# Optimization experiments

Measured on AMD Instinct MI355X. Metric: run time of the kernel, lower is better.

The kernel has to match this reference:

```python
import jax, jax.numpy as jnp
import numpy as np
import math

D_MODEL = 1024
N_HEADS = 16
HEAD_DIM = D_MODEL // N_HEADS
MLP_DIM = 4 * D_MODEL
B, L, M = 2, 2048, 2048


def layer_norm(x, g, b, eps=1e-5):
    mu = jnp.mean(x, axis=-1, keepdims=True)
    var = jnp.var(x, axis=-1, keepdims=True)
    return (x - mu) * jax.lax.rsqrt(var + eps) * g + b


def mha(q_in, k_in, qW, wW, oW, mask=None):
    # Faithful to source: k and v share w_proj, and the value einsum uses k.
    b, l, _ = q_in.shape
    m = k_in.shape[1]
    q = (q_in @ qW).reshape(b, l, HEAD_DIM, N_HEADS)
    k = (k_in @ wW).reshape(b, m, HEAD_DIM, N_HEADS)
    s = jnp.einsum('bldn,bmdn->blmn', q, k)
    if mask is not None:
        s = jnp.where(mask, -1e9, s)  # mask applied BEFORE scaling, as in source
    s = s / math.sqrt(HEAD_DIM)
    w = jax.nn.softmax(s, axis=2)
    x = jnp.einsum('blmn,bmdn->bldn', w, k)  # source bug: uses k, not v
    x = x.reshape(b, l, HEAD_DIM * N_HEADS)
    return x @ oW


def setup_inputs() -> dict:
    key = jax.random.key(0)
    ks = jax.random.split(key, 16)
    sc = 1.0 / math.sqrt(D_MODEL)
    inp = {
        'x': jax.random.normal(ks[0], (B, L, D_MODEL), jnp.float32),
        'enc_output': jax.random.normal(ks[1], (B, M, D_MODEL), jnp.float32),
        'mask': jax.random.randint(ks[2], (B, 1, M, 1), 0, 2).astype(bool),
        'q1W': jax.random.normal(ks[3], (D_MODEL, D_MODEL), jnp.float32) * sc,
        'w1W': jax.random.normal(ks[4], (D_MODEL, D_MODEL), jnp.float32) * sc,
        'o1W': jax.random.normal(ks[5], (D_MODEL, D_MODEL), jnp.float32) * sc,
        'q2W': jax.random.normal(ks[6], (D_MODEL, D_MODEL), jnp.float32) * sc,
        'w2W': jax.random.normal(ks[7], (D_MODEL, D_MODEL), jnp.float32) * sc,
        'o2W': jax.random.normal(ks[8], (D_MODEL, D_MODEL), jnp.float32) * sc,
        'ffW1': jax.random.normal(ks[9], (D_MODEL, MLP_DIM), jnp.float32) * sc,
        'ffb1': jnp.zeros((MLP_DIM,), jnp.float32),
        'ffW2': jax.random.normal(ks[10], (MLP_DIM, D_MODEL), jnp.float32) * sc,
        'ffb2': jnp.zeros((D_MODEL,), jnp.float32),
        'g1': jnp.ones((D_MODEL,), jnp.float32), 'b1': jnp.zeros((D_MODEL,), jnp.float32),
        'g2': jnp.ones((D_MODEL,), jnp.float32), 'b2': jnp.zeros((D_MODEL,), jnp.float32),
        'g3': jnp.ones((D_MODEL,), jnp.float32), 'b3': jnp.zeros((D_MODEL,), jnp.float32),
    }
    return inp


def reference(x, enc_output, mask, q1W, w1W, o1W, q2W, w2W, o2W,
              ffW1, ffb1, ffW2, ffb2, g1, b1, g2, b2, g3, b3):
    # self-attention (no mask, as in source)
    sa = mha(x, x, q1W, w1W, o1W, mask=None)
    x = layer_norm(x + sa, g1, b1)
    # encoder-decoder attention with mask
    ca = mha(x, enc_output, q2W, w2W, o2W, mask=mask)
    x = layer_norm(x + ca, g2, b2)
    # feed-forward (exact GELU, matching torch nn.GELU default)
    h = jax.nn.gelu(x @ ffW1 + ffb1, approximate=False)
    ff = h @ ffW2 + ffb2
    x = layer_norm(x + ff, g3, b3)
    return x
```

## Files before the change

kernel.cpp:

```cpp
#include <hip/hip_runtime.h>
#include <hip/hip_bf16.h>
#include <math.h>
#include <stdint.h>

typedef __attribute__((ext_vector_type(8))) short bf16x8_t;
typedef __attribute__((ext_vector_type(4))) float f32x4_t;

#define LOG2E 1.4426950408889634f
#define GLB(p) ((const __attribute__((address_space(1))) void*)(p))
#define LDS(p) ((__attribute__((address_space(3))) void*)(p))

__device__ __forceinline__ unsigned short f2bf(float f) {
    union { float f; unsigned int u; } v; v.f = f;
    unsigned int r = v.u + 0x7FFFu + ((v.u >> 16) & 1u);
    return (unsigned short)(r >> 16);
}

__device__ __forceinline__ float bf2f(unsigned short us) {
    union { unsigned int u; float f; } c; c.u = (unsigned int)us << 16; return c.f;
}

__device__ __forceinline__ unsigned int pack2bf(float a, float b) {
#if __has_builtin(__builtin_amdgcn_cvt_pk_bf16_f32)
    auto r = __builtin_amdgcn_cvt_pk_bf16_f32(a, b);
    unsigned int u;
    __builtin_memcpy(&u, &r, 4);
    return u;
#else
    return (unsigned int)f2bf(a) | ((unsigned int)f2bf(b) << 16);
#endif
}

__device__ __forceinline__ float fast_rcp(float x) {
#if __has_builtin(__builtin_amdgcn_rcpf)
    return __builtin_amdgcn_rcpf(x);
#else
    return 1.0f / x;
#endif
}

__device__ __forceinline__ float fexp2(float x) {
#if __has_builtin(__builtin_amdgcn_exp2f)
    return __builtin_amdgcn_exp2f(x);
#else
    return exp2f(x);
#endif
}

__device__ __forceinline__ float gelu_fast(float v) {
    float x2 = v * v;
    float inner = v * fmaf(0.0356774081f, x2, 0.7978845608f);
    inner = fminf(fmaxf(inner, -20.f), 20.f);
    float t = fexp2(inner * 2.8853900817779268f);
    return v * t * fast_rcp(t + 1.0f);
}

__global__ void cast2_bf16_k(const float* __restrict__ inA, unsigned short* __restrict__ outA,
                             const float* __restrict__ inB, unsigned short* __restrict__ outB,
                             int n4, const int* __restrict__ maskp, float* __restrict__ mask4) {
    if (blockIdx.y == 2) {
        int i = blockIdx.x * blockDim.x + threadIdx.x;
        if (i < 8192) {
            int nt = i & 3, l16 = (i >> 2) & 15, t = (i >> 6) & 31, b = (i >> 11) & 1;
            mask4[i] = maskp[b * 2048 + t * 64 + nt * 16 + l16] ? -1e10f : 0.0f;
        }
        return;
    }
    const float* in = blockIdx.y ? inB : inA;
    unsigned short* out = blockIdx.y ? outB : outA;
    int i = blockIdx.x * blockDim.x + threadIdx.x;
    if (i < n4) {
        float4 v = ((const float4*)in)[i];
        ushort4 o;
        o.x = f2bf(v.x); o.y = f2bf(v.y); o.z = f2bf(v.z); o.w = f2bf(v.w);
        ((ushort4*)out)[i] = o;
    }
}

__global__ void transpose_all_k(const float* __restrict__ s0, const float* __restrict__ s1,
                                const float* __restrict__ s2, const float* __restrict__ s3,
                                const float* __restrict__ s4, const float* __restrict__ s5,
                                const float* __restrict__ s6, const float* __restrict__ s7,
                                unsigned short* __restrict__ d0, unsigned short* __restrict__ d1,
                                unsigned short* __restrict__ d2, unsigned short* __restrict__ d3,
                                unsigned short* __restrict__ d4, unsigned short* __restrict__ d5,
                                unsigned short* __restrict__ d6, unsigned short* __restrict__ d7) {
    __shared__ float tile[32][33];
    int idx = blockIdx.x;
    const float* W; unsigned short* Wt; int K, N, bx, by;
    bool permK = false;
    if (idx < 6144) {
        int which = idx >> 10, t = idx & 1023;
        bx = t & 31; by = t >> 5; K = 1024; N = 1024;
        switch (which) {
            case 0: W = s0; Wt = d0; break;
            case 1: W = s1; Wt = d1; break;
            case 2: W = s2; Wt = d2; permK = true; break;
            case 3: W = s3; Wt = d3; break;
            case 4: W = s4; Wt = d4; break;
            default: W = s5; Wt = d5; permK = true; break;
        }
    } else if (idx < 10240) {
        int t = idx - 6144;
        bx = t & 127; by = t >> 7; K = 1024; N = 4096;
        W = s6; Wt = d6;
    } else {
        int t = idx - 10240;
        bx = t & 31; by = t >> 5; K = 4096; N = 1024;
        W = s7; Wt = d7;
    }
    int k0 = by * 32, n0 = bx * 32;
    int tx = threadIdx.x, ty = threadIdx.y;
#pragma unroll
    for (int i = 0; i < 32; i += 8) {
        int kr = k0 + ty + i;
        int srcr = permK ? ((kr & 63) * 16 + (kr >> 6)) : kr;
        tile[ty + i][tx] = W[(long)srcr * N + n0 + tx];
    }
    __syncthreads();
#pragma unroll
    for (int i = 0; i < 32; i += 8)
        Wt[(long)(n0 + ty + i) * K + k0 + tx] = f2bf(tile[tx][ty + i]);
}

template <int EP>
__global__ __launch_bounds__(512, 4) void gemm8_k(const unsigned short* __restrict__ A,
                                                  const unsigned short* __restrict__ Bt,
                                                  void* __restrict__ outp,
                                                  const float* __restrict__ bias,
                                                  const unsigned short* __restrict__ A2,
                                                  const unsigned short* __restrict__ Bt2,
                                                  unsigned short* __restrict__ qout,
                                                  unsigned short* __restrict__ kout,
                                                  unsigned short* __restrict__ ktout,
                                                  int M, int N, int K) {
    if (blockIdx.z) { A = A2; Bt = Bt2; }
    __shared__ __align__(16) unsigned short SMEM[32768];
    unsigned short* As = SMEM;
    unsigned short* Bs = SMEM + 16384;
    int tid = threadIdx.x;
    int wave = tid >> 6, lane = tid & 63;
    int wm = wave >> 2, wn = wave & 3;
    int quad = lane >> 4, l16 = lane & 15;
    int bm = blockIdx.y * 128, bn = blockIdx.x * 128;

    f32x4_t acc[4][2] = {};

    int srow = tid >> 3;
    int sgrp = (tid & 7) ^ (srow & 7);
    const unsigned short* Ag[2];
    const unsigned short* Bg[2];
#pragma unroll
    for (int i = 0; i < 2; i++) {
        Ag[i] = A + (long)(bm + i * 64 + srow) * K + sgrp * 8;
        Bg[i] = Bt + (long)(bn + i * 64 + srow) * K + sgrp * 8;
    }

    auto stage = [&](int buf, int k0) {
#pragma unroll
        for (int i = 0; i < 2; i++)
            __builtin_amdgcn_global_load_lds(GLB(Ag[i] + k0), LDS(As + buf * 8192 + i * 4096 + tid * 8), 16, 0, 0);
#pragma unroll
        for (int i = 0; i < 2; i++)
            __builtin_amdgcn_global_load_lds(GLB(Bg[i] + k0), LDS(Bs + buf * 8192 + i * 4096 + tid * 8), 16, 0, 0);
    };

    auto compute = [&](int buf) {
        const unsigned short* Ab = As + buf * 8192;
        const unsigned short* Bb = Bs + buf * 8192;
#pragma unroll
        for (int kk = 0; kk < 2; kk++) {
            int xg = ((kk * 4 + quad) ^ (l16 & 7)) * 8;
            bf16x8_t af[4], bfr[2];
#pragma unroll
            for (int t = 0; t < 4; t++)
                af[t] = *(const bf16x8_t*)(Ab + (wm * 64 + t * 16 + l16) * 64 + xg);
#pragma unroll
            for (int t = 0; t < 2; t++)
                bfr[t] = *(const bf16x8_t*)(Bb + (wn * 32 + t * 16 + l16) * 64 + xg);
#pragma unroll
            for (int mt = 0; mt < 4; mt++)
#pragma unroll
                for (int nt = 0; nt < 2; nt++)
                    acc[mt][nt] = __builtin_amdgcn_mfma_f32_16x16x32_bf16(af[mt], bfr[nt], acc[mt][nt], 0, 0, 0);
        }
    };

    stage(0, 0);
    const int NS = K >> 6;
    for (int i = 0; i < NS; i++) {
        if (i + 1 < NS) {
            stage((i + 1) & 1, (i + 1) << 6);
            asm volatile("s_waitcnt vmcnt(4)\n\ts_barrier" ::: "memory");
        } else {
            asm volatile("s_waitcnt vmcnt(0)\n\ts_barrier" ::: "memory");
        }
        compute(i & 1);
        asm volatile("s_barrier" ::: "memory");
    }

    if (EP == 7 || EP == 8) {
        bool kmode = (EP == 7) ? (bn >= 1024) : (blockIdx.z != 0);
        int G = (EP == 7 && kmode) ? ((bn - 1024) >> 7) : (bn >> 7);
        unsigned short* Ct = SMEM;
#pragma unroll
        for (int mt = 0; mt < 4; mt++)
#pragma unroll
            for (int nt = 0; nt < 2; nt++)
#pragma unroll
                for (int r = 0; r < 4; r++) {
                    int rr = wm * 64 + mt * 16 + quad * 4 + r;
                    int cc = wn * 32 + nt * 16 + l16;
                    Ct[rr * 132 + cc] = f2bf(acc[mt][nt][r]);
                }
        __syncthreads();
        int bq = bm >> 11;
        if (!kmode) {
#pragma unroll
            for (int i = 0; i < 4; i++) {
                int e = tid + i * 512;
                int h = e & 15, rl = e >> 4;
                int ll = (bm & 2047) + rl;
                union { uint4 v; unsigned short s[8]; } u;
#pragma unroll
                for (int j = 0; j < 8; j++) u.s[j] = Ct[rl * 132 + j * 16 + h];
                *(uint4*)(qout + (((long)(bq * 16 + h) * 2048 + ll) << 6) + ((G ^ (ll & 7)) << 3)) = u.v;
            }
        } else {
#pragma unroll
            for (int i = 0; i < 4; i++) {
                int e = tid + i * 512;
                int h = e & 15, rl = e >> 4;
                int mm = (bm & 2047) + rl;
                union { uint4 v; unsigned short s[8]; } u;
#pragma unroll
                for (int j = 0; j < 8; j++) u.s[j] = Ct[rl * 132 + j * 16 + h];
                *(uint4*)(kout + (((long)(bq * 16 + h) * 2048 + mm) << 6) + ((G ^ (mm & 7)) << 3)) = u.v;
            }
#pragma unroll
            for (int i = 0; i < 4; i++) {
                int e = tid + i * 512;
                int glog = e & 7, m0s = (e >> 3) & 1, dl = (e >> 4) & 7, h = e >> 7;
                int d = G * 8 + dl;
                union { uint4 v; unsigned short s[8]; } u;
#pragma unroll
                for (int j = 0; j < 8; j++) {
                    int p = glog * 8 + j;
                    int ml = (p >> 2) + (p & 3) * 16;
                    u.s[j] = Ct[(m0s * 64 + ml) * 132 + dl * 16 + h];
                }
                int mmbase = (bm & 2047) + m0s * 64;
                int gph = glog ^ (d & 7);
                *(uint4*)(ktout + ((long)(bq * 16 + h) * 64 + d) * 2048 + mmbase + gph * 8) = u.v;
            }
        }
        return;
    }

#pragma unroll
    for (int mt = 0; mt < 4; mt++)
#pragma unroll
        for (int nt = 0; nt < 2; nt++)
#pragma unroll
            for (int r = 0; r < 4; r++) {
                int gm = bm + wm * 64 + mt * 16 + quad * 4 + r;
                int gn = bn + wn * 32 + nt * 16 + l16;
                float v = acc[mt][nt][r];
                if (EP == 2) {
                    v = gelu_fast(v + bias[gn]);
                    ((unsigned short*)outp)[(long)gm * N + gn] = f2bf(v);
                } else if (EP == 6) {
                    ((unsigned short*)outp)[(long)gm * N + gn] = f2bf(v + bias[gn]);
                } else {
                    ((unsigned short*)outp)[(long)gm * N + gn] = f2bf(v);
                }
            }
}

template <int USE_MASK>
__global__ __launch_bounds__(256, 4) void flash_attn11_k(const unsigned short* __restrict__ Qh,
                                                         const unsigned short* __restrict__ Kh,
                                                         const unsigned short* __restrict__ KhTp,
                                                         const float* __restrict__ mask4,
                                                         unsigned short* __restrict__ out) {
    __shared__ __align__(16) unsigned short K1[64 * 64];
    __shared__ __align__(16) unsigned short K2[64 * 64];
    __shared__ __align__(16) unsigned short Ps[64 * 64];
    __shared__ __align__(16) float Ml[USE_MASK ? 2048 : 4];

    int tid = threadIdx.x;
    int wave = tid >> 6, lane = tid & 63;
    int quad = lane >> 4, l16 = lane & 15;
    int o = blockIdx.y * 32 + blockIdx.x;
    int bh = (o & 7) + ((o >> 8) << 3);
    int l0 = ((o >> 3) & 31) << 6;
    int b = bh >> 4, h = bh & 15;
    const unsigned short* k1p = Kh + (long)bh * 2048 * 64 + tid * 8;
    const unsigned short* k2p = KhTp + (long)bh * 64 * 2048 + (long)(tid >> 3) * 2048 + (tid & 7) * 8;

    int sw = l16 & 7;

    const unsigned short* qrow = Qh + ((long)bh * 2048 + l0 + wave * 16 + l16) * 64;
    bf16x8_t qf[2];
#pragma unroll
    for (int kk = 0; kk < 2; kk++)
        qf[kk] = *(const bf16x8_t*)(qrow + ((kk * 4 + quad) ^ sw) * 8);

    __builtin_amdgcn_global_load_lds(GLB(k1p), LDS(K1 + tid * 8), 16, 0, 0);
    __builtin_amdgcn_global_load_lds(GLB(k1p + 2048), LDS(K1 + tid * 8 + 2048), 16, 0, 0);
    __builtin_amdgcn_global_load_lds(GLB(k2p), LDS(K2 + tid * 8), 16, 0, 0);
    __builtin_amdgcn_global_load_lds(GLB(k2p + 32 * 2048), LDS(K2 + tid * 8 + 2048), 16, 0, 0);
    if (USE_MASK) {
        const float* mp = mask4 + b * 2048;
        for (int c = tid; c < 512; c += 256)
            ((float4*)Ml)[c] = ((const float4*)mp)[c];
    }
    __syncthreads();

    const float C1 = 0.125f * LOG2E;
    f32x4_t acc_o[4] = {};
    float rs[4] = {0.f, 0.f, 0.f, 0.f};

    for (int t = 0; t < 32; ++t) {
        uint4 rA, rB, rC, rD;
        if (t < 31) {
            k1p += 4096;
            k2p += 64;
            rA = *(const uint4*)(k1p);
            rB = *(const uint4*)(k1p + 2048);
            rC = *(const uint4*)(k2p);
            rD = *(const uint4*)(k2p + 32 * 2048);
        }

        float4 mq = make_float4(0.f, 0.f, 0.f, 0.f);
        if (USE_MASK) mq = *(const float4*)(Ml + t * 64 + l16 * 4);

        f32x4_t sacc[4] = {};
        __builtin_amdgcn_s_setprio(1);
#pragma unroll
        for (int kk = 0; kk < 2; kk++) {
            int xg = ((kk * 4 + quad) ^ sw) * 8;
#pragma unroll
            for (int nt = 0; nt < 4; nt++) {
                bf16x8_t bfr = *(const bf16x8_t*)(K1 + (nt * 16 + l16) * 64 + xg);
                sacc[nt] = __builtin_amdgcn_mfma_f32_16x16x32_bf16(qf[kk], bfr, sacc[nt], 0, 0, 0);
            }
        }
        __builtin_amdgcn_s_setprio(0);

#pragma unroll
        for (int r = 0; r < 4; r++) {
            float p0 = fexp2(fmaf(sacc[0][r], C1, mq.x));
            float p1 = fexp2(fmaf(sacc[1][r], C1, mq.y));
            float p2 = fexp2(fmaf(sacc[2][r], C1, mq.z));
            float p3 = fexp2(fmaf(sacc[3][r], C1, mq.w));
            rs[r] += (p0 + p1) + (p2 + p3);
            uint2 pk; pk.x = pack2bf(p0, p1); pk.y = pack2bf(p2, p3);
            int Rrow = wave * 16 + quad * 4 + r;
            int grp = (l16 >> 1) ^ (Rrow & 7);
            *(uint2*)(Ps + Rrow * 64 + grp * 8 + (l16 & 1) * 4) = pk;
        }

        __builtin_amdgcn_s_setprio(1);
#pragma unroll
        for (int kk = 0; kk < 2; kk++) {
            int xg = ((kk * 4 + quad) ^ sw) * 8;
            int Rr = wave * 16 + l16;
            int pg = ((kk * 4 + quad) ^ (l16 & 7)) * 8;
            bf16x8_t af = *(const bf16x8_t*)(Ps + Rr * 64 + pg);
#pragma unroll
            for (int nt = 0; nt < 4; nt++) {
                bf16x8_t bfr = *(const bf16x8_t*)(K2 + (nt * 16 + l16) * 64 + xg);
                acc_o[nt] = __builtin_amdgcn_mfma_f32_16x16x32_bf16(af, bfr, acc_o[nt], 0, 0, 0);
            }
        }
        __builtin_amdgcn_s_setprio(0);

        asm volatile("s_barrier" ::: "memory");
        if (t < 31) {
            *(uint4*)(K1 + tid * 8) = rA;
            *(uint4*)(K1 + tid * 8 + 2048) = rB;
            *(uint4*)(K2 + tid * 8) = rC;
            *(uint4*)(K2 + tid * 8 + 2048) = rD;
            asm volatile("s_waitcnt lgkmcnt(0)\n\ts_barrier" ::: "memory");
        }
    }

#pragma unroll
    for (int r = 0; r < 4; r++) {
#pragma unroll
        for (int d = 1; d < 16; d <<= 1) rs[r] += __shfl_xor(rs[r], d);
    }

#pragma unroll
    for (int r = 0; r < 4; r++) {
        float inv = 1.0f / rs[r];
        int l = l0 + wave * 16 + quad * 4 + r;
#pragma unroll
        for (int nt = 0; nt < 4; nt++) {
            int d = nt * 16 + l16;
            out[((long)(b * 2048 + l)) * 1024 + h * 64 + d] = f2bf(acc_o[nt][r] * inv);
        }
    }
}

template <int AIN_BF16, int OUT_F32>
__global__ __launch_bounds__(256) void resid_ln_k(const void* __restrict__ ap,
                                                  const unsigned short* __restrict__ rb,
                                                  const float* __restrict__ g,
                                                  const float* __restrict__ bb,
                                                  float* __restrict__ outf,
                                                  unsigned short* __restrict__ outb) {
    long row = blockIdx.x;
    int tid = threadIdx.x;
    float x0, x1, x2, x3;
    if (AIN_BF16) {
        ushort4 va = ((const ushort4*)((const unsigned short*)ap + row * 1024))[tid];
        x0 = bf2f(va.x); x1 = bf2f(va.y); x2 = bf2f(va.z); x3 = bf2f(va.w);
    } else {
        float4 va = ((const float4*)((const float*)ap + row * 1024))[tid];
        x0 = va.x; x1 = va.y; x2 = va.z; x3 = va.w;
    }
    ushort4 vr = ((const ushort4*)(rb + row * 1024))[tid];
    x0 += bf2f(vr.x); x1 += bf2f(vr.y); x2 += bf2f(vr.z); x3 += bf2f(vr.w);
    float s = x0 + x1 + x2 + x3;
    float sq = x0 * x0 + x1 * x1 + x2 * x2 + x3 * x3;
#pragma unroll
    for (int d = 1; d < 64; d <<= 1) { s += __shfl_xor(s, d); sq += __shfl_xor(sq, d); }
    __shared__ float ss[4], ssq[4];
    int wave = tid >> 6, lane = tid & 63;
    if (lane == 0) { ss[wave] = s; ssq[wave] = sq; }
    __syncthreads();
    s = ss[0] + ss[1] + ss[2] + ss[3];
    sq = ssq[0] + ssq[1] + ssq[2] + ssq[3];
    float mean = s * (1.0f / 1024.0f);
    float var = sq * (1.0f / 1024.0f) - mean * mean;
    float rstd = rsqrtf(var + 1e-5f);
    float4 vg = ((const float4*)g)[tid];
    float4 vb = ((const float4*)bb)[tid];
    float y0 = (x0 - mean) * rstd * vg.x + vb.x;
    float y1 = (x1 - mean) * rstd * vg.y + vb.y;
    float y2 = (x2 - mean) * rstd * vg.z + vb.z;
    float y3 = (x3 - mean) * rstd * vg.w + vb.w;
    if (OUT_F32) {
        float4 o; o.x = y0; o.y = y1; o.z = y2; o.w = y3;
        ((float4*)(outf + row * 1024))[tid] = o;
    } else {
        ushort4 ob; ob.x = f2bf(y0); ob.y = f2bf(y1); ob.z = f2bf(y2); ob.w = f2bf(y3);
        ((ushort4*)(outb + row * 1024))[tid] = ob;
    }
}

extern "C" void kernel_launch(void* const* d_in, const int* in_sizes, int n_in,
                              void* d_out, int out_size, void* d_ws, size_t ws_size,
                              hipStream_t stream) {
    const float* x    = (const float*)d_in[0];
    const float* enc  = (const float*)d_in[1];
    const int*   mask = (const int*)d_in[2];
    const float* q1W  = (const float*)d_in[3];
    const float* w1W  = (const float*)d_in[4];
    const float* o1W  = (const float*)d_in[5];
    const float* q2W  = (const float*)d_in[6];
    const float* w2W  = (const float*)d_in[7];
    const float* o2W  = (const float*)d_in[8];
    const float* ffW1 = (const float*)d_in[9];
    const float* ffb1 = (const float*)d_in[10];
    const float* ffW2 = (const float*)d_in[11];
    const float* ffb2 = (const float*)d_in[12];
    const float* g1 = (const float*)d_in[13];
    const float* b1 = (const float*)d_in[14];
    const float* g2 = (const float*)d_in[15];
    const float* b2 = (const float*)d_in[16];
    const float* g3 = (const float*)d_in[17];
    const float* b3 = (const float*)d_in[18];
    float* outp = (float*)d_out;

    const int T = 4096;
    const int D = 1024;
    const int F = 4096;

    char* ws = (char*)d_ws;
    auto alloc = [&](size_t sz) { char* p = ws; ws += (sz + 255) & ~(size_t)255; return p; };
    unsigned short* qw1Wt = (unsigned short*)alloc((size_t)2 * D * D * 2);
    unsigned short* o1Wt  = (unsigned short*)alloc((size_t)D * D * 2);
    unsigned short* q2Wt  = (unsigned short*)alloc((size_t)D * D * 2);
    unsigned short* w2Wt  = (unsigned short*)alloc((size_t)D * D * 2);
    unsigned short* o2Wt  = (unsigned short*)alloc((size_t)D * D * 2);
    unsigned short* ffW1t = (unsigned short*)alloc((size_t)F * D * 2);
    unsigned short* ffW2t = (unsigned short*)alloc((size_t)D * F * 2);
    unsigned short* xb    = (unsigned short*)alloc((size_t)T * D * 2);
    unsigned short* encb  = (unsigned short*)alloc((size_t)T * D * 2);
    unsigned short* Qhb   = (unsigned short*)alloc((size_t)T * D * 2);
    unsigned short* Khb   = (unsigned short*)alloc((size_t)T * D * 2);
    unsigned short* KhTb  = (unsigned short*)alloc((size_t)T * D * 2);
    unsigned short* attnb = (unsigned short*)alloc((size_t)T * D * 2);
    float*          mask4b= (float*)alloc((size_t)8192 * 4);
    unsigned short* projb = (unsigned short*)alloc((size_t)T * D * 2);
    unsigned short* x1s   = (unsigned short*)alloc((size_t)T * D * 2);
    unsigned short* x2s   = (unsigned short*)alloc((size_t)T * D * 2);
    unsigned short* S1    = (unsigned short*)alloc((size_t)T * F * 2);
    unsigned short* hb    = S1;

    dim3 blk256(256);
    dim3 blk512(512);
    dim3 tblk(32, 8);

    cast2_bf16_k<<<dim3(T * D / 4 / 256, 3), blk256, 0, stream>>>(x, xb, enc, encb, T * D / 4, mask, mask4b);
    transpose_all_k<<<dim3(14336), tblk, 0, stream>>>(
        q1W, w1W, o1W, q2W, w2W, o2W, ffW1, ffW2,
        qw1Wt, qw1Wt + (size_t)D * D, o1Wt, q2Wt, w2Wt, o2Wt, ffW1t, ffW2t);

    gemm8_k<7><<<dim3(2 * D / 128, T / 128, 1), blk512, 0, stream>>>(
        xb, qw1Wt, nullptr, nullptr, nullptr, nullptr, Qhb, Khb, KhTb, T, 2 * D, D);
    flash_attn11_k<0><<<dim3(32, 32), blk256, 0, stream>>>(Qhb, Khb, KhTb, nullptr, attnb);
    gemm8_k<4><<<dim3(D / 128, T / 128, 1), blk512, 0, stream>>>(
        attnb, o1Wt, projb, nullptr, nullptr, nullptr, nullptr, nullptr, nullptr, T, D, D);
    resid_ln_k<0, 0><<<dim3(T), blk256, 0, stream>>>(x, projb, g1, b1, nullptr, x1s);

    gemm8_k<8><<<dim3(D / 128, T / 128, 2), blk512, 0, stream>>>(
        x1s, q2Wt, nullptr, nullptr, encb, w2Wt, Qhb, Khb, KhTb, T, D, D);
    flash_attn11_k<1><<<dim3(32, 32), blk256, 0, stream>>>(Qhb, Khb, KhTb, mask4b, attnb);
    gemm8_k<4><<<dim3(D / 128, T / 128, 1), blk512, 0, stream>>>(
        attnb, o2Wt, projb, nullptr, nullptr, nullptr, nullptr, nullptr, nullptr, T, D, D);
    resid_ln_k<1, 0><<<dim3(T), blk256, 0, stream>>>(x1s, projb, g2, b2, nullptr, x2s);

    gemm8_k<2><<<dim3(F / 128, T / 128, 1), blk512, 0, stream>>>(
        x2s, ffW1t, hb, ffb1, nullptr, nullptr, nullptr, nullptr, nullptr, T, F, D);
    gemm8_k<6><<<dim3(D / 128, T / 128, 1), blk512, 0, stream>>>(
        hb, ffW2t, projb, ffb2, nullptr, nullptr, nullptr, nullptr, nullptr, T, D, F);
    resid_ln_k<1, 1><<<dim3(T), blk256, 0, stream>>>(x2s, projb, g3, b3, outp, nullptr);
}
```

Measured before the change: 479.3 us.

## Double-buffer K tiles in flash attention and pack mask into bitfields

The attention kernel now keeps two LDS buffers for the K and K-transposed tiles. Each iteration writes the next prefetched tile into the idle buffer and computes on the current one, which replaces two barriers per iteration with one. The key mask is packed into 32-bit words per column group and held in registers, so the LDS mask array and its per-iteration load go away. LDS usage grows by 16KB per block, which may reduce occupancy.

```diff
diff --git a/kernel.cpp b/kernel.cpp
--- a/kernel.cpp
+++ b/kernel.cpp
@@ -57,12 +57,15 @@
 
 __global__ void cast2_bf16_k(const float* __restrict__ inA, unsigned short* __restrict__ outA,
                              const float* __restrict__ inB, unsigned short* __restrict__ outB,
-                             int n4, const int* __restrict__ maskp, float* __restrict__ mask4) {
+                             int n4, const int* __restrict__ maskp, unsigned int* __restrict__ maskbits) {
     if (blockIdx.y == 2) {
         int i = blockIdx.x * blockDim.x + threadIdx.x;
-        if (i < 8192) {
-            int nt = i & 3, l16 = (i >> 2) & 15, t = (i >> 6) & 31, b = (i >> 11) & 1;
-            mask4[i] = maskp[b * 2048 + t * 64 + nt * 16 + l16] ? -1e10f : 0.0f;
+        if (i < 128) {
+            int nt = i & 3, l16 = (i >> 2) & 15, b = i >> 6;
+            unsigned int w = 0;
+            for (int t = 0; t < 32; t++)
+                w |= (maskp[b * 2048 + t * 64 + nt * 16 + l16] ? 1u : 0u) << t;
+            maskbits[i] = w;
         }
         return;
     }
@@ -278,15 +281,14 @@
 }
 
 template <int USE_MASK>
-__global__ __launch_bounds__(256, 4) void flash_attn11_k(const unsigned short* __restrict__ Qh,
+__global__ __launch_bounds__(256, 4) void flash_attn12_k(const unsigned short* __restrict__ Qh,
                                                          const unsigned short* __restrict__ Kh,
                                                          const unsigned short* __restrict__ KhTp,
-                                                         const float* __restrict__ mask4,
+                                                         const unsigned int* __restrict__ maskbits,
                                                          unsigned short* __restrict__ out) {
-    __shared__ __align__(16) unsigned short K1[64 * 64];
-    __shared__ __align__(16) unsigned short K2[64 * 64];
+    __shared__ __align__(16) unsigned short K1[2 * 64 * 64];
+    __shared__ __align__(16) unsigned short K2[2 * 64 * 64];
     __shared__ __align__(16) unsigned short Ps[64 * 64];
-    __shared__ __align__(16) float Ml[USE_MASK ? 2048 : 4];
 
     int tid = threadIdx.x;
     int wave = tid >> 6, lane = tid & 63;
@@ -306,34 +308,56 @@
     for (int kk = 0; kk < 2; kk++)
         qf[kk] = *(const bf16x8_t*)(qrow + ((kk * 4 + quad) ^ sw) * 8);
 
+    uint4 mb = make_uint4(0, 0, 0, 0);
+    if (USE_MASK) mb = *(const uint4*)(maskbits + (b * 16 + l16) * 4);
+
     __builtin_amdgcn_global_load_lds(GLB(k1p), LDS(K1 + tid * 8), 16, 0, 0);
     __builtin_amdgcn_global_load_lds(GLB(k1p + 2048), LDS(K1 + tid * 8 + 2048), 16, 0, 0);
     __builtin_amdgcn_global_load_lds(GLB(k2p), LDS(K2 + tid * 8), 16, 0, 0);
     __builtin_amdgcn_global_load_lds(GLB(k2p + 32 * 2048), LDS(K2 + tid * 8 + 2048), 16, 0, 0);
-    if (USE_MASK) {
-        const float* mp = mask4 + b * 2048;
-        for (int c = tid; c < 512; c += 256)
-            ((float4*)Ml)[c] = ((const float4*)mp)[c];
-    }
     __syncthreads();
+
+    k1p += 4096;
+    k2p += 64;
+    uint4 rA = *(const uint4*)(k1p);
+    uint4 rB = *(const uint4*)(k1p + 2048);
+    uint4 rC = *(const uint4*)(k2p);
+    uint4 rD = *(const uint4*)(k2p + 32 * 2048);
 
     const float C1 = 0.125f * LOG2E;
     f32x4_t acc_o[4] = {};
     float rs[4] = {0.f, 0.f, 0.f, 0.f};
 
     for (int t = 0; t < 32; ++t) {
-        uint4 rA, rB, rC, rD;
+        int cur = t & 1;
+        asm volatile("s_barrier" ::: "memory");
         if (t < 31) {
-            k1p += 4096;
-            k2p += 64;
-            rA = *(const uint4*)(k1p);
-            rB = *(const uint4*)(k1p + 2048);
-            rC = *(const uint4*)(k2p);
-            rD = *(const uint4*)(k2p + 32 * 2048);
-        }
-
-        float4 mq = make_float4(0.f, 0.f, 0.f, 0.f);
-        if (USE_MASK) mq = *(const float4*)(Ml + t * 64 + l16 * 4);
+            unsigned short* K1n = K1 + ((cur ^ 1) << 12);
+            unsigned short* K2n = K2 + ((cur ^ 1) << 12);
+            *(uint4*)(K1n + tid * 8) = rA;
+            *(uint4*)(K1n + tid * 8 + 2048) = rB;
+            *(uint4*)(K2n + tid * 8) = rC;
+            *(uint4*)(K2n + tid * 8 + 2048) = rD;
+            if (t < 30) {
+                k1p += 4096;
+                k2p += 64;
+                rA = *(const uint4*)(k1p);
+                rB = *(const uint4*)(k1p + 2048);
+                rC = *(const uint4*)(k2p);
+                rD = *(const uint4*)(k2p + 32 * 2048);
+            }
+        }
+        const unsigned short* K1c = K1 + (cur << 12);
+        const unsigned short* K2c = K2 + (cur << 12);
+
+        float mqx = 0.f, mqy = 0.f, mqz = 0.f, mqw = 0.f;
+        if (USE_MASK) {
+            unsigned int bit = 1u << t;
+            mqx = (mb.x & bit) ? -1e10f : 0.0f;
+            mqy = (mb.y & bit) ? -1e10f : 0.0f;
+            mqz = (mb.z & bit) ? -1e10f : 0.0f;
+            mqw = (mb.w & bit) ? -1e10f : 0.0f;
+        }
 
         f32x4_t sacc[4] = {};
         __builtin_amdgcn_s_setprio(1);
@@ -342,7 +366,7 @@
             int xg = ((kk * 4 + quad) ^ sw) * 8;
 #pragma unroll
             for (int nt = 0; nt < 4; nt++) {
-                bf16x8_t bfr = *(const bf16x8_t*)(K1 + (nt * 16 + l16) * 64 + xg);
+                bf16x8_t bfr = *(const bf16x8_t*)(K1c + (nt * 16 + l16) * 64 + xg);
                 sacc[nt] = __builtin_amdgcn_mfma_f32_16x16x32_bf16(qf[kk], bfr, sacc[nt], 0, 0, 0);
             }
         }
@@ -350,10 +374,10 @@
 
 #pragma unroll
         for (int r = 0; r < 4; r++) {
-            float p0 = fexp2(fmaf(sacc[0][r], C1, mq.x));
-            float p1 = fexp2(fmaf(sacc[1][r], C1, mq.y));
-            float p2 = fexp2(fmaf(sacc[2][r], C1, mq.z));
-            float p3 = fexp2(fmaf(sacc[3][r], C1, mq.w));
+            float p0 = fexp2(fmaf(sacc[0][r], C1, mqx));
+            float p1 = fexp2(fmaf(sacc[1][r], C1, mqy));
+            float p2 = fexp2(fmaf(sacc[2][r], C1, mqz));
+            float p3 = fexp2(fmaf(sacc[3][r], C1, mqw));
             rs[r] += (p0 + p1) + (p2 + p3);
             uint2 pk; pk.x = pack2bf(p0, p1); pk.y = pack2bf(p2, p3);
             int Rrow = wave * 16 + quad * 4 + r;
@@ -370,20 +394,11 @@
             bf16x8_t af = *(const bf16x8_t*)(Ps + Rr * 64 + pg);
 #pragma unroll
             for (int nt = 0; nt < 4; nt++) {
-                bf16x8_t bfr = *(const bf16x8_t*)(K2 + (nt * 16 + l16) * 64 + xg);
+                bf16x8_t bfr = *(const bf16x8_t*)(K2c + (nt * 16 + l16) * 64 + xg);
                 acc_o[nt] = __builtin_amdgcn_mfma_f32_16x16x32_bf16(af, bfr, acc_o[nt], 0, 0, 0);
             }
         }
         __builtin_amdgcn_s_setprio(0);
-
-        asm volatile("s_barrier" ::: "memory");
-        if (t < 31) {
-            *(uint4*)(K1 + tid * 8) = rA;
-            *(uint4*)(K1 + tid * 8 + 2048) = rB;
-            *(uint4*)(K2 + tid * 8) = rC;
-            *(uint4*)(K2 + tid * 8 + 2048) = rD;
-            asm volatile("s_waitcnt lgkmcnt(0)\n\ts_barrier" ::: "memory");
-        }
     }
 
 #pragma unroll
@@ -494,7 +509,7 @@
     unsigned short* Khb   = (unsigned short*)alloc((size_t)T * D * 2);
     unsigned short* KhTb  = (unsigned short*)alloc((size_t)T * D * 2);
     unsigned short* attnb = (unsigned short*)alloc((size_t)T * D * 2);
-    float*          mask4b= (float*)alloc((size_t)8192 * 4);
+    unsigned int*   maskbb= (unsigned int*)alloc((size_t)128 * 4);
     unsigned short* projb = (unsigned short*)alloc((size_t)T * D * 2);
     unsigned short* x1s   = (unsigned short*)alloc((size_t)T * D * 2);
     unsigned short* x2s   = (unsigned short*)alloc((size_t)T * D * 2);
@@ -505,21 +520,21 @@
     dim3 blk512(512);
     dim3 tblk(32, 8);
 
-    cast2_bf16_k<<<dim3(T * D / 4 / 256, 3), blk256, 0, stream>>>(x, xb, enc, encb, T * D / 4, mask, mask4b);
+    cast2_bf16_k<<<dim3(T * D / 4 / 256, 3), blk256, 0, stream>>>(x, xb, enc, encb, T * D / 4, mask, maskbb);
     transpose_all_k<<<dim3(14336), tblk, 0, stream>>>(
         q1W, w1W, o1W, q2W, w2W, o2W, ffW1, ffW2,
         qw1Wt, qw1Wt + (size_t)D * D, o1Wt, q2Wt, w2Wt, o2Wt, ffW1t, ffW2t);
 
     gemm8_k<7><<<dim3(2 * D / 128, T / 128, 1), blk512, 0, stream>>>(
         xb, qw1Wt, nullptr, nullptr, nullptr, nullptr, Qhb, Khb, KhTb, T, 2 * D, D);
-    flash_attn11_k<0><<<dim3(32, 32), blk256, 0, stream>>>(Qhb, Khb, KhTb, nullptr, attnb);
+    flash_attn12_k<0><<<dim3(32, 32), blk256, 0, stream>>>(Qhb, Khb, KhTb, nullptr, attnb);
     gemm8_k<4><<<dim3(D / 128, T / 128, 1), blk512, 0, stream>>>(
         attnb, o1Wt, projb, nullptr, nullptr, nullptr, nullptr, nullptr, nullptr, T, D, D);
     resid_ln_k<0, 0><<<dim3(T), blk256, 0, stream>>>(x, projb, g1, b1, nullptr, x1s);
 
     gemm8_k<8><<<dim3(D / 128, T / 128, 2), blk512, 0, stream>>>(
         x1s, q2Wt, nullptr, nullptr, encb, w2Wt, Qhb, Khb, KhTb, T, D, D);
-    flash_attn11_k<1><<<dim3(32, 32), blk256, 0, stream>>>(Qhb, Khb, KhTb, mask4b, attnb);
+    flash_attn12_k<1><<<dim3(32, 32), blk256, 0, stream>>>(Qhb, Khb, KhTb, maskbb, attnb);
     gemm8_k<4><<<dim3(D / 128, T / 128, 1), blk512, 0, stream>>>(
         attnb, o2Wt, projb, nullptr, nullptr, nullptr, nullptr, nullptr, nullptr, T, D, D);
     resid_ln_k<1, 0><<<dim3(T), blk256, 0, stream>>>(x1s, projb, g2, b2, nullptr, x2s);
```

Measured after the change: 500.3 us. +4.4%, slower.
